# Performance work log

Hardware: AMD Instinct MI355X
Metric: run time of the kernel (lower is better)

The kernel has to match this reference:

```python
import jax, jax.numpy as jnp
import numpy as np
from jax import lax

# ---- configuration (matches init_kwargs) ----
DH = 4.0        # grid_spacing (m)
DT = 0.0008     # time step (s), satisfies CFL for vmax=2600
PML = 20        # pml_width (cells, all four edges)
VMAX = 2600.0   # max_vel used for PML profile
PAD = 2         # halo for 4th-order (accuracy=4) stencil


def _shift(wp, k, axis, n):
    return lax.slice_in_dim(wp, PAD + k, PAD + k + n, axis=axis)


def _d1(w, axis, dh):
    # 4th-order first derivative: (-f[+2] + 8 f[+1] - 8 f[-1] + f[-2]) / (12 h)
    n = w.shape[axis]
    pad = [(0, 0)] * w.ndim
    pad[axis] = (PAD, PAD)
    wp = jnp.pad(w, pad)
    return ((_shift(wp, -2, axis, n) - _shift(wp, 2, axis, n))
            + 8.0 * (_shift(wp, 1, axis, n) - _shift(wp, -1, axis, n))) / (12.0 * dh)


def _d2(w, axis, dh):
    # 4th-order second derivative: (-f[+-2] + 16 f[+-1] - 30 f[0]) / (12 h^2)
    n = w.shape[axis]
    pad = [(0, 0)] * w.ndim
    pad[axis] = (PAD, PAD)
    wp = jnp.pad(w, pad)
    return (-(_shift(wp, -2, axis, n) + _shift(wp, 2, axis, n))
            + 16.0 * (_shift(wp, 1, axis, n) + _shift(wp, -1, axis, n))
            - 30.0 * w) / (12.0 * dh * dh)


def _pml_profiles(n, pml, dh, dt, vmax):
    # CPML absorption profiles: sigma ~ quadratic ramp into the PML,
    # b = exp(-sigma*dt), a = b - 1 (kappa=1, alpha=0)
    sigma_max = np.float32(3.0 * vmax * np.log(1000.0) / (2.0 * pml * dh))
    x = jnp.arange(n, dtype=jnp.float32)
    d = jnp.maximum(jnp.clip((pml - x) / pml, 0.0, 1.0),
                    jnp.clip((x - (n - 1 - pml)) / pml, 0.0, 1.0))
    sigma = sigma_max * d * d
    b = jnp.exp(-sigma * dt)
    return b - 1.0, b


def setup_inputs() -> dict:
    key = jax.random.key(0)
    k1, k2, k3, k4 = jax.random.split(key, 4)
    ny = nx = 400
    B, n_src, n_rec, nt = 4, 1, 100, 100
    v = 1500.0 + 1000.0 * jax.random.uniform(k1, (ny, nx), dtype=jnp.float32)
    source_amplitudes = jax.random.normal(k2, (B, n_src, nt), dtype=jnp.float32)
    source_locations = jax.random.randint(k3, (B, n_src, 2), 40, 360).astype(jnp.int64)
    receiver_locations = jax.random.randint(k4, (B, n_rec, 2), 40, 360).astype(jnp.int64)
    return {"v": v, "source_amplitudes": source_amplitudes,
            "source_locations": source_locations,
            "receiver_locations": receiver_locations}


def reference(v, source_amplitudes, source_locations, receiver_locations):
    B, n_src, nt = source_amplitudes.shape
    # replicate edge velocities into the PML region (as deepwave does)
    vp = jnp.pad(v, ((PML, PML), (PML, PML)), mode="edge")
    NY, NX = vp.shape
    v2dt2 = (vp * vp) * (DT * DT)          # [NY, NX]
    ay, by = _pml_profiles(NY, PML, DH, DT, VMAX)
    ax, bx = _pml_profiles(NX, PML, DH, DT, VMAX)
    ay, by = ay[None, :, None], by[None, :, None]
    ax, bx = ax[None, None, :], bx[None, None, :]

    sy = source_locations[..., 0] + PML    # [B, n_src]
    sx = source_locations[..., 1] + PML
    ry = receiver_locations[..., 0] + PML  # [B, n_rec]
    rx = receiver_locations[..., 1] + PML
    bidx = jnp.arange(B)[:, None]
    src_scale = v2dt2[sy, sx]              # [B, n_src]

    zero = jnp.zeros((B, NY, NX), v.dtype)
    carry0 = (zero, zero, zero, zero, zero, zero)

    def step(carry, amp_t):
        wfc, wfm, psiy, psix, zetay, zetax = carry
        # PML memory variables for first derivatives
        psiy = by * psiy + ay * _d1(wfc, 1, DH)
        psix = bx * psix + ax * _d1(wfc, 2, DH)
        # PML-corrected second derivatives
        d2y = _d2(wfc, 1, DH) + _d1(psiy, 1, DH)
        d2x = _d2(wfc, 2, DH) + _d1(psix, 2, DH)
        zetay = by * zetay + ay * d2y
        zetax = bx * zetax + ax * d2x
        # explicit leapfrog time step
        wfp = v2dt2[None] * (d2y + zetay + d2x + zetax) + 2.0 * wfc - wfm
        # inject sources scaled by v^2 dt^2 (as deepwave)
        wfp = wfp.at[bidx, sy, sx].add(src_scale * amp_t)
        rec = wfp[bidx, ry, rx]            # [B, n_rec]
        return (wfp, wfc, psiy, psix, zetay, zetax), rec

    amps_t = jnp.moveaxis(source_amplitudes, 2, 0)  # [nt, B, n_src]
    _, recs = lax.scan(step, carry0, amps_t)        # recs: [nt, B, n_rec]
    receiver_amplitudes = jnp.moveaxis(recs, 0, 2)  # [B, n_rec, nt]
    return receiver_amplitudes
```

## Files before the change

kernel.cpp:

```cpp
#include <hip/hip_runtime.h>

#define NVEL  400
#define PMLW  20
#define NSIDE 440
#define BATCH 4
#define NT    100
#define NREC  100

#define TS 55
#define GT 8
#define WP 68
#define WROWS 63
#define WHALF (WROWS*WP)
#define PYP 56
#define PXP 60
#define C1f (1.0f/48.0f)
#define C2f (1.0f/192.0f)
#define NTH 1024
#define NSTRIP 880
#define SPITCH (256*NSTRIP)

typedef float f4 __attribute__((ext_vector_type(4)));
#define F4(x) (*(f4*)&(x))
#define WIDX(y,x) (((y)+4)*WP + ((x)+4))

__global__ __launch_bounds__(NTH, 1) void kWave(
    const float* __restrict__ v, const float* __restrict__ amp,
    const int* __restrict__ sloc, const int* __restrict__ rloc,
    float* __restrict__ out, int* __restrict__ flags, float* __restrict__ strips)
{
    __shared__ __align__(16) float sWF[2*WHALF];
    __shared__ __align__(16) float sPY[59*PYP];
    __shared__ __align__(16) float sPX[TS*PXP];
    __shared__ float pa_y[63], pb_y[63], pa_x[63], pb_x[63];
    __shared__ float sAmp[NT];

    const int tid = threadIdx.x;
    const int bid = blockIdx.x;
    const int b   = bid >> 6;
    const int tl  = bid & 63;
    const int tyi = tl >> 3, txi = tl & 7;
    const int by0 = tyi*TS, bx0 = txi*TS;
    const int nbN = (tyi > 0)    ? bid - GT : -1;
    const int nbS = (tyi < GT-1) ? bid + GT : -1;
    const int nbW = (txi > 0)    ? bid - 1  : -1;
    const int nbE = (txi < GT-1) ? bid + 1  : -1;

    for (int i = tid; i < 2*WHALF; i += NTH) sWF[i] = 0.f;
    for (int i = tid; i < 59*PYP; i += NTH) sPY[i] = 0.f;
    for (int i = tid; i < TS*PXP; i += NTH) sPX[i] = 0.f;
    if (tid < 63) {
        const float smax = (float)(3.0*2600.0*6.907755278982137/160.0);
        float gy = (float)(by0 + tid - 4);
        float dy = fmaxf(fminf(fmaxf((20.f-gy)/20.f,0.f),1.f),
                         fminf(fmaxf((gy-419.f)/20.f,0.f),1.f));
        float bby = expf(-smax*dy*dy*0.0008f);
        pb_y[tid] = bby; pa_y[tid] = bby - 1.f;
        float gx = (float)(bx0 + tid - 4);
        float dx = fmaxf(fminf(fmaxf((20.f-gx)/20.f,0.f),1.f),
                         fminf(fmaxf((gx-419.f)/20.f,0.f),1.f));
        float bbx = expf(-smax*dx*dx*0.0008f);
        pb_x[tid] = bbx; pa_x[tid] = bbx - 1.f;
    }
    if (tid < NT) sAmp[tid] = amp[b*NT + tid];
    __syncthreads();

    const bool pyOn = (tid < 826);
    const int  pyRi = tid/14, pyQx = (tid - 14*pyRi)*4;
    const bool pyCore = pyOn && (pyRi >= 4 && pyRi <= 54);
    const bool pyRim  = pyOn && !(pyRi >= 4 && pyRi <= 54);
    const int  pyWf  = pyRi*WP + (pyQx+4);
    const int  pyIdx = pyRi*PYP + pyQx;
    float pyPa = 0.f, pyPb = 0.f;
    if (pyOn) { int g = by0 + pyRi - 2;
        if (g >= 0 && g < NSIDE) { pyPa = pa_y[pyRi+2]; pyPb = pb_y[pyRi+2]; } }

    const bool pxOn = (tid < 825);
    const int  pxY = tid/15, pxQ = tid - 15*pxY, pxJ = pxQ*4;
    const bool pxCore = pxOn && (pxQ >= 1 && pxQ <= 12);
    const bool pxRim  = pxOn && !(pxQ >= 1 && pxQ <= 12);
    const int  pxWf  = (pxY+4)*WP + pxJ;
    const int  pxIdx = pxY*PXP + pxJ;
    f4 pxPa, pxPb;
    pxPa.x=0.f;pxPa.y=0.f;pxPa.z=0.f;pxPa.w=0.f;
    pxPb.x=0.f;pxPb.y=0.f;pxPb.z=0.f;pxPb.w=0.f;
    if (pxOn) {
        int g0 = bx0 + pxJ - 2;
        if (g0+0 >= 0 && g0+0 < NSIDE) { pxPa.x = pa_x[pxJ+2]; pxPb.x = pb_x[pxJ+2]; }
        if (g0+1 >= 0 && g0+1 < NSIDE) { pxPa.y = pa_x[pxJ+3]; pxPb.y = pb_x[pxJ+3]; }
        if (g0+2 >= 0 && g0+2 < NSIDE) { pxPa.z = pa_x[pxJ+4]; pxPb.z = pb_x[pxJ+4]; }
        if (g0+3 >= 0 && g0+3 < NSIDE) { pxPa.w = pa_x[pxJ+5]; pxPb.w = pb_x[pxJ+5]; }
    }

    const bool inOn = (tid < 770);
    const int  iY = tid/14, iQ = tid - 14*iY, iQx = iQ*4;
    const bool iTail = (iQ == 13);
    const int  iC  = WIDX(iY, iQx);
    const int  iPy = iY*PYP + iQx;
    const int  iPx = iY*PXP + iQx;
    const float iPay = pa_y[iY+4], iPby = pb_y[iY+4];
    f4 iPax, iPbx, iV2, iSrc;
    {
        iPax.x = pa_x[iQx+4]; iPax.y = pa_x[iQx+5]; iPax.z = pa_x[iQx+6]; iPax.w = pa_x[iQx+7];
        iPbx.x = pb_x[iQx+4]; iPbx.y = pb_x[iQx+5]; iPbx.z = pb_x[iQx+6]; iPbx.w = pb_x[iQx+7];
        const int sgy = sloc[b*2] + PMLW, sgx = sloc[b*2+1] + PMLW;
        int cy = min(max(by0 + iY - PMLW, 0), NVEL-1);
        #pragma unroll
        for (int e = 0; e < 4; ++e) {
            int cx = min(max(bx0 + iQx + e - PMLW, 0), NVEL-1);
            float vv = v[cy*NVEL + cx];
            float v2 = vv*vv*(float)(0.0008*0.0008);
            float sm = (inOn && (by0+iY == sgy) && (bx0+iQx+e == sgx)) ? v2 : 0.f;
            if (e==0) { iV2.x=v2; iSrc.x=sm; } else if (e==1) { iV2.y=v2; iSrc.y=sm; }
            else if (e==2) { iV2.z=v2; iSrc.z=sm; } else { iV2.w=v2; iSrc.w=sm; }
        }
    }
    f4 zY, zX;
    zY.x=0.f;zY.y=0.f;zY.z=0.f;zY.w=0.f;
    zX.x=0.f;zX.y=0.f;zX.z=0.f;zX.w=0.f;

    int rofs = -1, rIdx = 0;
    if (tid < NREC) {
        int gry = rloc[(b*NREC+tid)*2]   + PMLW;
        int grx = rloc[(b*NREC+tid)*2+1] + PMLW;
        if (gry >= by0 && gry < by0+TS && grx >= bx0 && grx < bx0+TS) {
            rofs = (b*NREC+tid)*NT;
            rIdx = WIDX(gry-by0, grx-bx0);
        }
    }

    int impNb = -1, imSrc = 0, imDst = 0;
    int exSrc = 0;
    if (tid < NSTRIP) {
        int e = tid/220, j = tid - e*220;
        if (e == 0)      { int r=j/55, c=j-55*r; impNb=nbN; imSrc=1*220+j; imDst=WIDX(r-4,c);  exSrc=WIDX(r,c); }
        else if (e == 1) { int r=j/55, c=j-55*r; impNb=nbS; imSrc=0*220+j; imDst=WIDX(55+r,c); exSrc=WIDX(51+r,c); }
        else if (e == 2) { int r=j&3,  c=j>>2;   impNb=nbW; imSrc=3*220+j; imDst=WIDX(c,r-4);  exSrc=WIDX(c,r); }
        else             { int r=j&3,  c=j>>2;   impNb=nbE; imSrc=2*220+j; imDst=WIDX(c,55+r); exSrc=WIDX(c,51+r); }
        if (impNb >= 0) imSrc += impNb*NSTRIP;
    }
    __syncthreads();

    int co = 0;

#define PSIY_BODY { \
    f4 r0 = F4(sWF[co+pyWf]);      f4 r1 = F4(sWF[co+pyWf+WP]); \
    f4 r3 = F4(sWF[co+pyWf+3*WP]); f4 r4 = F4(sWF[co+pyWf+4*WP]); \
    f4 po = F4(sPY[pyIdx]); f4 nv; \
    nv.x = pyPb*po.x + pyPa*((r0.x - r4.x + 8.f*(r3.x - r1.x))*C1f); \
    nv.y = pyPb*po.y + pyPa*((r0.y - r4.y + 8.f*(r3.y - r1.y))*C1f); \
    nv.z = pyPb*po.z + pyPa*((r0.z - r4.z + 8.f*(r3.z - r1.z))*C1f); \
    nv.w = pyPb*po.w + pyPa*((r0.w - r4.w + 8.f*(r3.w - r1.w))*C1f); \
    F4(sPY[pyIdx]) = nv; }

#define PSIX_BODY { \
    f4 L = F4(sWF[co+pxWf]); f4 R = F4(sWF[co+pxWf+4]); \
    f4 po = F4(sPX[pxIdx]); f4 nv; \
    nv.x = pxPb.x*po.x + pxPa.x*((L.x - R.x + 8.f*(L.w - L.y))*C1f); \
    nv.y = pxPb.y*po.y + pxPa.y*((L.y - R.y + 8.f*(R.x - L.z))*C1f); \
    nv.z = pxPb.z*po.z + pxPa.z*((L.z - R.z + 8.f*(R.y - L.w))*C1f); \
    nv.w = pxPb.w*po.w + pxPa.w*((L.w - R.w + 8.f*(R.z - R.x))*C1f); \
    F4(sPX[pxIdx]) = nv; }

    for (int t = 0; t < NT; ++t) {
        float hval = 0.f;
        if (t > 0 && impNb >= 0) {
            int spin = 0;
            while (__hip_atomic_load(&flags[impNb], __ATOMIC_RELAXED,
                                     __HIP_MEMORY_SCOPE_AGENT) < t
                   && spin < 2000000) { __builtin_amdgcn_s_sleep(1); ++spin; }
            hval = __hip_atomic_load(&strips[((t-1)&1)*SPITCH + imSrc],
                                     __ATOMIC_RELAXED, __HIP_MEMORY_SCOPE_AGENT);
        }
        asm volatile("" ::: "memory");

        if (pyCore) PSIY_BODY;
        if (pxCore) PSIX_BODY;

        if (t > 0 && impNb >= 0) sWF[co+imDst] = hval;
        __syncthreads();

        if (pyRim) PSIY_BODY;
        if (pxRim) PSIX_BODY;
        __syncthreads();

        if (inOn) {
            const int cn = co ^ WHALF;
            f4 Cc  = F4(sWF[co+iC]);
            f4 ym2 = F4(sWF[co+iC-2*WP]), ym1 = F4(sWF[co+iC-WP]);
            f4 yp1 = F4(sWF[co+iC+WP]),   yp2 = F4(sWF[co+iC+2*WP]);
            f4 xl  = F4(sWF[co+iC-4]),    xr  = F4(sWF[co+iC+4]);
            f4 p0 = F4(sPY[iPy]),         p1 = F4(sPY[iPy+PYP]);
            f4 p3 = F4(sPY[iPy+3*PYP]),   p4 = F4(sPY[iPy+4*PYP]);
            f4 pl = F4(sPX[iPx]),         pr = F4(sPX[iPx+4]);
            f4 n4 = F4(sWF[cn+iC]);
            const float ampT = sAmp[t];

            float d2y, d2x, w0, w1, w2, w3;
            d2y = (-(ym2.x+yp2.x) + 16.f*(ym1.x+yp1.x) - 30.f*Cc.x)*C2f
                + (p0.x - p4.x + 8.f*(p3.x - p1.x))*C1f;
            d2x = (-(xl.z + Cc.z) + 16.f*(xl.w + Cc.y) - 30.f*Cc.x)*C2f
                + (pl.x - pr.x + 8.f*(pl.w - pl.y))*C1f;
            zY.x = iPby*zY.x + iPay*d2y;
            zX.x = iPbx.x*zX.x + iPax.x*d2x;
            w0 = iV2.x*(d2y + zY.x + d2x + zX.x) + 2.f*Cc.x - n4.x + iSrc.x*ampT;
            d2y = (-(ym2.y+yp2.y) + 16.f*(ym1.y+yp1.y) - 30.f*Cc.y)*C2f
                + (p0.y - p4.y + 8.f*(p3.y - p1.y))*C1f;
            d2x = (-(xl.w + Cc.w) + 16.f*(Cc.x + Cc.z) - 30.f*Cc.y)*C2f
                + (pl.y - pr.y + 8.f*(pr.x - pl.z))*C1f;
            zY.y = iPby*zY.y + iPay*d2y;
            zX.y = iPbx.y*zX.y + iPax.y*d2x;
            w1 = iV2.y*(d2y + zY.y + d2x + zX.y) + 2.f*Cc.y - n4.y + iSrc.y*ampT;
            d2y = (-(ym2.z+yp2.z) + 16.f*(ym1.z+yp1.z) - 30.f*Cc.z)*C2f
                + (p0.z - p4.z + 8.f*(p3.z - p1.z))*C1f;
            d2x = (-(Cc.x + xr.x) + 16.f*(Cc.y + Cc.w) - 30.f*Cc.z)*C2f
                + (pl.z - pr.z + 8.f*(pr.y - pl.w))*C1f;
            zY.z = iPby*zY.z + iPay*d2y;
            zX.z = iPbx.z*zX.z + iPax.z*d2x;
            w2 = iV2.z*(d2y + zY.z + d2x + zX.z) + 2.f*Cc.z - n4.z + iSrc.z*ampT;
            d2y = (-(ym2.w+yp2.w) + 16.f*(ym1.w+yp1.w) - 30.f*Cc.w)*C2f
                + (p0.w - p4.w + 8.f*(p3.w - p1.w))*C1f;
            d2x = (-(Cc.y + xr.y) + 16.f*(Cc.z + xr.x) - 30.f*Cc.w)*C2f
                + (pl.w - pr.w + 8.f*(pr.z - pr.x))*C1f;
            zY.w = iPby*zY.w + iPay*d2y;
            zX.w = iPbx.w*zX.w + iPax.w*d2x;
            w3 = iV2.w*(d2y + zY.w + d2x + zX.w) + 2.f*Cc.w - n4.w + iSrc.w*ampT;

            if (!iTail) {
                f4 w4; w4.x = w0; w4.y = w1; w4.z = w2; w4.w = w3;
                F4(sWF[cn+iC]) = w4;
            } else {
                sWF[cn+iC] = w0; sWF[cn+iC+1] = w1; sWF[cn+iC+2] = w2;
            }
        }
        __syncthreads();

        const int cn = co ^ WHALF;
        if (rofs >= 0) out[rofs + t] = sWF[cn + rIdx];
        if (t < NT-1 && tid < NSTRIP) {
            __hip_atomic_store(&strips[(t&1)*SPITCH + bid*NSTRIP + tid],
                               sWF[cn + exSrc], __ATOMIC_RELAXED,
                               __HIP_MEMORY_SCOPE_AGENT);
        }
        __builtin_amdgcn_s_waitcnt(0);
        __syncthreads();
        if (t < NT-1 && tid == 0)
            __hip_atomic_store(&flags[bid], t+1, __ATOMIC_RELEASE,
                               __HIP_MEMORY_SCOPE_AGENT);

        co ^= WHALF;
    }
#undef PSIY_BODY
#undef PSIX_BODY
}

extern "C" void kernel_launch(void* const* d_in, const int* in_sizes, int n_in,
                              void* d_out, int out_size, void* d_ws, size_t ws_size,
                              hipStream_t stream) {
    const float* v    = (const float*)d_in[0];
    const float* amp  = (const float*)d_in[1];
    const int*   sloc = (const int*)d_in[2];
    const int*   rloc = (const int*)d_in[3];
    float* out = (float*)d_out;

    int*   flags  = (int*)d_ws;
    float* strips = (float*)((char*)d_ws + 1024);

    hipMemsetAsync(flags, 0, 1024, stream);
    kWave<<<256, NTH, 0, stream>>>(v, amp, sloc, rloc, out, flags, strips);
}
```

Measured before the change: 832.9 us.

## Overlap interior wavefield update with halo wait and export strips from registers

The per-step schedule is reordered. Core PML memory updates now run first. The interior wavefield points that do not depend on neighbour halos are then updated while halo values are still being fetched from neighbouring blocks, and rim points are computed after the halo lands. Halo strips are written to global memory straight from the computed registers, with a padded slot layout, instead of being read back from shared memory in a separate phase. This aims to hide inter-block synchronisation latency, at the cost of an extra barrier per step and scattered scalar atomic stores.

```diff
diff --git a/kernel.cpp b/kernel.cpp
--- a/kernel.cpp
+++ b/kernel.cpp
@@ -17,8 +17,9 @@
 #define C1f (1.0f/48.0f)
 #define C2f (1.0f/192.0f)
 #define NTH 1024
-#define NSTRIP 880
-#define SPITCH (256*NSTRIP)
+#define SLOTP 224
+#define BSTRIP 896
+#define SPITCH (256*BSTRIP)
 
 typedef float f4 __attribute__((ext_vector_type(4)));
 #define F4(x) (*(f4*)&(x))
@@ -95,6 +96,8 @@
     const bool inOn = (tid < 770);
     const int  iY = tid/14, iQ = tid - 14*iY, iQx = iQ*4;
     const bool iTail = (iQ == 13);
+    const bool iCore = inOn && (iY >= 4 && iY <= 50) && (iQ >= 1 && iQ <= 12);
+    const bool iRim  = inOn && !iCore;
     const int  iC  = WIDX(iY, iQx);
     const int  iPy = iY*PYP + iQx;
     const int  iPx = iY*PXP + iQx;
@@ -119,6 +122,15 @@
     zY.x=0.f;zY.y=0.f;zY.z=0.f;zY.w=0.f;
     zX.x=0.f;zX.y=0.f;zX.z=0.f;zX.w=0.f;
 
+    int exN=-1, exS=-1, exW=-1, exE12=-1, exE13=-1;
+    if (inOn) {
+        if (tyi > 0    && iY < 4)   exN = bid*BSTRIP + 0*SLOTP + iY*56 + iQx;
+        if (tyi < GT-1 && iY >= 51) exS = bid*BSTRIP + 1*SLOTP + (iY-51)*56 + iQx;
+        if (txi > 0    && iQ == 0)  exW = bid*BSTRIP + 2*SLOTP + iY*4;
+        if (txi < GT-1 && iQ == 12) exE12 = bid*BSTRIP + 3*SLOTP + iY*4;
+        if (txi < GT-1 && iQ == 13) exE13 = bid*BSTRIP + 3*SLOTP + iY*4;
+    }
+
     int rofs = -1, rIdx = 0;
     if (tid < NREC) {
         int gry = rloc[(b*NREC+tid)*2]   + PMLW;
@@ -130,14 +142,13 @@
     }
 
     int impNb = -1, imSrc = 0, imDst = 0;
-    int exSrc = 0;
-    if (tid < NSTRIP) {
+    if (tid < 880) {
         int e = tid/220, j = tid - e*220;
-        if (e == 0)      { int r=j/55, c=j-55*r; impNb=nbN; imSrc=1*220+j; imDst=WIDX(r-4,c);  exSrc=WIDX(r,c); }
-        else if (e == 1) { int r=j/55, c=j-55*r; impNb=nbS; imSrc=0*220+j; imDst=WIDX(55+r,c); exSrc=WIDX(51+r,c); }
-        else if (e == 2) { int r=j&3,  c=j>>2;   impNb=nbW; imSrc=3*220+j; imDst=WIDX(c,r-4);  exSrc=WIDX(c,r); }
-        else             { int r=j&3,  c=j>>2;   impNb=nbE; imSrc=2*220+j; imDst=WIDX(c,55+r); exSrc=WIDX(c,51+r); }
-        if (impNb >= 0) imSrc += impNb*NSTRIP;
+        if (e == 0)      { int r=j/55, c=j-55*r; impNb=nbN; imSrc=1*SLOTP + r*56 + c; imDst=WIDX(r-4,c); }
+        else if (e == 1) { int r=j/55, c=j-55*r; impNb=nbS; imSrc=0*SLOTP + r*56 + c; imDst=WIDX(55+r,c); }
+        else if (e == 2) { int r=j&3,  c=j>>2;   impNb=nbW; imSrc=3*SLOTP + c*4 + r;  imDst=WIDX(c,r-4); }
+        else             { int r=j&3,  c=j>>2;   impNb=nbE; imSrc=2*SLOTP + c*4 + r;  imDst=WIDX(c,55+r); }
+        if (impNb >= 0) imSrc += impNb*BSTRIP;
     }
     __syncthreads();
 
@@ -162,7 +173,86 @@
     nv.w = pxPb.w*po.w + pxPa.w*((L.w - R.w + 8.f*(R.z - R.x))*C1f); \
     F4(sPX[pxIdx]) = nv; }
 
+#define INTERIOR_BODY { \
+    const int cn = co ^ WHALF; \
+    f4 Cc  = F4(sWF[co+iC]); \
+    f4 ym2 = F4(sWF[co+iC-2*WP]), ym1 = F4(sWF[co+iC-WP]); \
+    f4 yp1 = F4(sWF[co+iC+WP]),   yp2 = F4(sWF[co+iC+2*WP]); \
+    f4 xl  = F4(sWF[co+iC-4]),    xr  = F4(sWF[co+iC+4]); \
+    f4 p0 = F4(sPY[iPy]),         p1 = F4(sPY[iPy+PYP]); \
+    f4 p3 = F4(sPY[iPy+3*PYP]),   p4 = F4(sPY[iPy+4*PYP]); \
+    f4 pl = F4(sPX[iPx]),         pr = F4(sPX[iPx+4]); \
+    f4 n4 = F4(sWF[cn+iC]); \
+    const float ampT = sAmp[t]; \
+    float d2y, d2x, w0, w1, w2, w3; \
+    d2y = (-(ym2.x+yp2.x) + 16.f*(ym1.x+yp1.x) - 30.f*Cc.x)*C2f \
+        + (p0.x - p4.x + 8.f*(p3.x - p1.x))*C1f; \
+    d2x = (-(xl.z + Cc.z) + 16.f*(xl.w + Cc.y) - 30.f*Cc.x)*C2f \
+        + (pl.x - pr.x + 8.f*(pl.w - pl.y))*C1f; \
+    zY.x = iPby*zY.x + iPay*d2y; \
+    zX.x = iPbx.x*zX.x + iPax.x*d2x; \
+    w0 = iV2.x*(d2y + zY.x + d2x + zX.x) + 2.f*Cc.x - n4.x + iSrc.x*ampT; \
+    d2y = (-(ym2.y+yp2.y) + 16.f*(ym1.y+yp1.y) - 30.f*Cc.y)*C2f \
+        + (p0.y - p4.y + 8.f*(p3.y - p1.y))*C1f; \
+    d2x = (-(xl.w + Cc.w) + 16.f*(Cc.x + Cc.z) - 30.f*Cc.y)*C2f \
+        + (pl.y - pr.y + 8.f*(pr.x - pl.z))*C1f; \
+    zY.y = iPby*zY.y + iPay*d2y; \
+    zX.y = iPbx.y*zX.y + iPax.y*d2x; \
+    w1 = iV2.y*(d2y + zY.y + d2x + zX.y) + 2.f*Cc.y - n4.y + iSrc.y*ampT; \
+    d2y = (-(ym2.z+yp2.z) + 16.f*(ym1.z+yp1.z) - 30.f*Cc.z)*C2f \
+        + (p0.z - p4.z + 8.f*(p3.z - p1.z))*C1f; \
+    d2x = (-(Cc.x + xr.x) + 16.f*(Cc.y + Cc.w) - 30.f*Cc.z)*C2f \
+        + (pl.z - pr.z + 8.f*(pr.y - pl.w))*C1f; \
+    zY.z = iPby*zY.z + iPay*d2y; \
+    zX.z = iPbx.z*zX.z + iPax.z*d2x; \
+    w2 = iV2.z*(d2y + zY.z + d2x + zX.z) + 2.f*Cc.z - n4.z + iSrc.z*ampT; \
+    d2y = (-(ym2.w+yp2.w) + 16.f*(ym1.w+yp1.w) - 30.f*Cc.w)*C2f \
+        + (p0.w - p4.w + 8.f*(p3.w - p1.w))*C1f; \
+    d2x = (-(Cc.y + xr.y) + 16.f*(Cc.z + xr.x) - 30.f*Cc.w)*C2f \
+        + (pl.w - pr.w + 8.f*(pr.z - pr.x))*C1f; \
+    zY.w = iPby*zY.w + iPay*d2y; \
+    zX.w = iPbx.w*zX.w + iPax.w*d2x; \
+    w3 = iV2.w*(d2y + zY.w + d2x + zX.w) + 2.f*Cc.w - n4.w + iSrc.w*ampT; \
+    if (!iTail) { \
+        f4 w4v; w4v.x = w0; w4v.y = w1; w4v.z = w2; w4v.w = w3; \
+        F4(sWF[cn+iC]) = w4v; \
+    } else { \
+        sWF[cn+iC] = w0; sWF[cn+iC+1] = w1; sWF[cn+iC+2] = w2; \
+    } \
+    if (t < NT-1) { \
+        float* sp = strips + (t&1)*SPITCH; \
+        if (exN >= 0) { \
+            __hip_atomic_store(&sp[exN+0], w0, __ATOMIC_RELAXED, __HIP_MEMORY_SCOPE_AGENT); \
+            __hip_atomic_store(&sp[exN+1], w1, __ATOMIC_RELAXED, __HIP_MEMORY_SCOPE_AGENT); \
+            __hip_atomic_store(&sp[exN+2], w2, __ATOMIC_RELAXED, __HIP_MEMORY_SCOPE_AGENT); \
+            __hip_atomic_store(&sp[exN+3], w3, __ATOMIC_RELAXED, __HIP_MEMORY_SCOPE_AGENT); \
+        } \
+        if (exS >= 0) { \
+            __hip_atomic_store(&sp[exS+0], w0, __ATOMIC_RELAXED, __HIP_MEMORY_SCOPE_AGENT); \
+            __hip_atomic_store(&sp[exS+1], w1, __ATOMIC_RELAXED, __HIP_MEMORY_SCOPE_AGENT); \
+            __hip_atomic_store(&sp[exS+2], w2, __ATOMIC_RELAXED, __HIP_MEMORY_SCOPE_AGENT); \
+            __hip_atomic_store(&sp[exS+3], w3, __ATOMIC_RELAXED, __HIP_MEMORY_SCOPE_AGENT); \
+        } \
+        if (exW >= 0) { \
+            __hip_atomic_store(&sp[exW+0], w0, __ATOMIC_RELAXED, __HIP_MEMORY_SCOPE_AGENT); \
+            __hip_atomic_store(&sp[exW+1], w1, __ATOMIC_RELAXED, __HIP_MEMORY_SCOPE_AGENT); \
+            __hip_atomic_store(&sp[exW+2], w2, __ATOMIC_RELAXED, __HIP_MEMORY_SCOPE_AGENT); \
+            __hip_atomic_store(&sp[exW+3], w3, __ATOMIC_RELAXED, __HIP_MEMORY_SCOPE_AGENT); \
+        } \
+        if (exE12 >= 0) \
+            __hip_atomic_store(&sp[exE12], w3, __ATOMIC_RELAXED, __HIP_MEMORY_SCOPE_AGENT); \
+        if (exE13 >= 0) { \
+            __hip_atomic_store(&sp[exE13+1], w0, __ATOMIC_RELAXED, __HIP_MEMORY_SCOPE_AGENT); \
+            __hip_atomic_store(&sp[exE13+2], w1, __ATOMIC_RELAXED, __HIP_MEMORY_SCOPE_AGENT); \
+            __hip_atomic_store(&sp[exE13+3], w2, __ATOMIC_RELAXED, __HIP_MEMORY_SCOPE_AGENT); \
+        } \
+    } }
+
     for (int t = 0; t < NT; ++t) {
+        if (pyCore) PSIY_BODY;
+        if (pxCore) PSIX_BODY;
+        __syncthreads();
+
         float hval = 0.f;
         if (t > 0 && impNb >= 0) {
             int spin = 0;
@@ -173,10 +263,7 @@
                                      __ATOMIC_RELAXED, __HIP_MEMORY_SCOPE_AGENT);
         }
         asm volatile("" ::: "memory");
-
-        if (pyCore) PSIY_BODY;
-        if (pxCore) PSIX_BODY;
-
+        if (iCore) INTERIOR_BODY;
         if (t > 0 && impNb >= 0) sWF[co+imDst] = hval;
         __syncthreads();
 
@@ -184,64 +271,10 @@
         if (pxRim) PSIX_BODY;
         __syncthreads();
 
-        if (inOn) {
-            const int cn = co ^ WHALF;
-            f4 Cc  = F4(sWF[co+iC]);
-            f4 ym2 = F4(sWF[co+iC-2*WP]), ym1 = F4(sWF[co+iC-WP]);
-            f4 yp1 = F4(sWF[co+iC+WP]),   yp2 = F4(sWF[co+iC+2*WP]);
-            f4 xl  = F4(sWF[co+iC-4]),    xr  = F4(sWF[co+iC+4]);
-            f4 p0 = F4(sPY[iPy]),         p1 = F4(sPY[iPy+PYP]);
-            f4 p3 = F4(sPY[iPy+3*PYP]),   p4 = F4(sPY[iPy+4*PYP]);
-            f4 pl = F4(sPX[iPx]),         pr = F4(sPX[iPx+4]);
-            f4 n4 = F4(sWF[cn+iC]);
-            const float ampT = sAmp[t];
-
-            float d2y, d2x, w0, w1, w2, w3;
-            d2y = (-(ym2.x+yp2.x) + 16.f*(ym1.x+yp1.x) - 30.f*Cc.x)*C2f
-                + (p0.x - p4.x + 8.f*(p3.x - p1.x))*C1f;
-            d2x = (-(xl.z + Cc.z) + 16.f*(xl.w + Cc.y) - 30.f*Cc.x)*C2f
-                + (pl.x - pr.x + 8.f*(pl.w - pl.y))*C1f;
-            zY.x = iPby*zY.x + iPay*d2y;
-            zX.x = iPbx.x*zX.x + iPax.x*d2x;
-            w0 = iV2.x*(d2y + zY.x + d2x + zX.x) + 2.f*Cc.x - n4.x + iSrc.x*ampT;
-            d2y = (-(ym2.y+yp2.y) + 16.f*(ym1.y+yp1.y) - 30.f*Cc.y)*C2f
-                + (p0.y - p4.y + 8.f*(p3.y - p1.y))*C1f;
-            d2x = (-(xl.w + Cc.w) + 16.f*(Cc.x + Cc.z) - 30.f*Cc.y)*C2f
-                + (pl.y - pr.y + 8.f*(pr.x - pl.z))*C1f;
-            zY.y = iPby*zY.y + iPay*d2y;
-            zX.y = iPbx.y*zX.y + iPax.y*d2x;
-            w1 = iV2.y*(d2y + zY.y + d2x + zX.y) + 2.f*Cc.y - n4.y + iSrc.y*ampT;
-            d2y = (-(ym2.z+yp2.z) + 16.f*(ym1.z+yp1.z) - 30.f*Cc.z)*C2f
-                + (p0.z - p4.z + 8.f*(p3.z - p1.z))*C1f;
-            d2x = (-(Cc.x + xr.x) + 16.f*(Cc.y + Cc.w) - 30.f*Cc.z)*C2f
-                + (pl.z - pr.z + 8.f*(pr.y - pl.w))*C1f;
-            zY.z = iPby*zY.z + iPay*d2y;
-            zX.z = iPbx.z*zX.z + iPax.z*d2x;
-            w2 = iV2.z*(d2y + zY.z + d2x + zX.z) + 2.f*Cc.z - n4.z + iSrc.z*ampT;
-            d2y = (-(ym2.w+yp2.w) + 16.f*(ym1.w+yp1.w) - 30.f*Cc.w)*C2f
-                + (p0.w - p4.w + 8.f*(p3.w - p1.w))*C1f;
-            d2x = (-(Cc.y + xr.y) + 16.f*(Cc.z + xr.x) - 30.f*Cc.w)*C2f
-                + (pl.w - pr.w + 8.f*(pr.z - pr.x))*C1f;
-            zY.w = iPby*zY.w + iPay*d2y;
-            zX.w = iPbx.w*zX.w + iPax.w*d2x;
-            w3 = iV2.w*(d2y + zY.w + d2x + zX.w) + 2.f*Cc.w - n4.w + iSrc.w*ampT;
-
-            if (!iTail) {
-                f4 w4; w4.x = w0; w4.y = w1; w4.z = w2; w4.w = w3;
-                F4(sWF[cn+iC]) = w4;
-            } else {
-                sWF[cn+iC] = w0; sWF[cn+iC+1] = w1; sWF[cn+iC+2] = w2;
-            }
-        }
-        __syncthreads();
-
-        const int cn = co ^ WHALF;
-        if (rofs >= 0) out[rofs + t] = sWF[cn + rIdx];
-        if (t < NT-1 && tid < NSTRIP) {
-            __hip_atomic_store(&strips[(t&1)*SPITCH + bid*NSTRIP + tid],
-                               sWF[cn + exSrc], __ATOMIC_RELAXED,
-                               __HIP_MEMORY_SCOPE_AGENT);
-        }
+        if (iRim) INTERIOR_BODY;
+        __syncthreads();
+
+        if (rofs >= 0) out[rofs + t] = sWF[(co^WHALF) + rIdx];
         __builtin_amdgcn_s_waitcnt(0);
         __syncthreads();
         if (t < NT-1 && tid == 0)
@@ -252,6 +285,7 @@
     }
 #undef PSIY_BODY
 #undef PSIX_BODY
+#undef INTERIOR_BODY
 }
 
 extern "C" void kernel_launch(void* const* d_in, const int* in_sizes, int n_in,
```

Measured after the change: 843.8 us. About the same (+1.3%).
